# Performance work log

Measured on AMD Instinct MI355X. Metric: run time of the kernel, lower is better.

Reference implementation:

```python
import jax, jax.numpy as jnp
import numpy as np

N, H, E, T = 100000, 128, 500000, 6  # nodes, hidden, max edges, edge types


def setup_inputs() -> dict:
    key = jax.random.key(0)
    ks = jax.random.split(key, 16)
    xav_e = float(np.sqrt(6.0 / (H + T * H)))  # xavier_uniform for edge_dense
    xav_h = float(np.sqrt(6.0 / (H + H)))
    u = lambda k, s, a: jax.random.uniform(k, s, jnp.float32, -a, a)
    return {
        "node_embeddings": jax.random.normal(ks[0], (N, H), jnp.float32),
        "W_edge": u(ks[1], (H, T * H), xav_e),
        "b_edge": 1e-6 * jax.random.normal(ks[2], (T * H,), jnp.float32),
        "W_ir": u(ks[3], (H, H), xav_h), "b_ir": jnp.zeros((H,), jnp.float32),
        "W_iz": u(ks[4], (H, H), xav_h), "b_iz": jnp.zeros((H,), jnp.float32),
        "W_in": u(ks[5], (H, H), xav_h), "b_in": jnp.zeros((H,), jnp.float32),
        "W_hr": u(ks[6], (H, H), xav_h),
        "W_hz": u(ks[7], (H, H), xav_h),
        "W_hn": u(ks[8], (H, H), xav_h), "b_hn": jnp.zeros((H,), jnp.float32),
        "source_indices": jax.random.randint(ks[9], (E,), 0, N, jnp.int32),
        "dest_indices": jax.random.randint(ks[10], (E,), 0, N, jnp.int32),
        "edge_types": jax.random.randint(ks[11], (E,), 0, T, jnp.int32),
        "num_edges": 450000,
    }


def reference(node_embeddings, W_edge, b_edge, W_ir, b_ir, W_iz, b_iz,
              W_in, b_in, W_hr, W_hz, W_hn, b_hn,
              source_indices, dest_indices, edge_types, num_edges):
    num_nodes, hidden = node_embeddings.shape
    max_edges = edge_types.shape[0]
    # gather source nodes, project to all edge types at once: [E, T*H]
    src = node_embeddings[source_indices]
    all_types = (src @ W_edge + b_edge).reshape(max_edges, -1, hidden)  # [E,T,H]
    # select per-edge type
    msg = jnp.take_along_axis(all_types, edge_types[:, None, None], axis=1)[:, 0, :]
    # mask padding edges, scatter-add into destination nodes
    msg = jnp.where((jnp.arange(max_edges) < num_edges)[:, None], msg, 0)
    agg = jax.ops.segment_sum(msg, dest_indices, num_segments=num_nodes)
    # GRU update: carry h = aggregated messages, inputs x = node_embeddings
    h, x = agg, node_embeddings
    r = jax.nn.sigmoid(x @ W_ir + b_ir + h @ W_hr)
    z = jax.nn.sigmoid(x @ W_iz + b_iz + h @ W_hz)
    n = jnp.tanh(x @ W_in + b_in + r * (h @ W_hn + b_hn))
    return (1.0 - z) * n + z * h
```

## Files before the change

kernel.cpp:

```cpp
#include <hip/hip_runtime.h>
#include <hip/hip_bf16.h>

#define HD 128
#define NT 6

typedef unsigned short u16;
typedef unsigned int u32;
typedef __attribute__((ext_vector_type(8))) short bf16x8;
typedef __attribute__((ext_vector_type(4))) float f32x4;

__device__ __forceinline__ float sigmoidf_(float x) {
  return 1.0f / (1.0f + __expf(-x));
}

__device__ __forceinline__ u16 f2bf(float x) {
  u32 u = __float_as_uint(x);
  return (u16)((u + 0x7FFFu + ((u >> 16) & 1u)) >> 16);
}
__device__ __forceinline__ float bflo(u32 v) { return __uint_as_float(v << 16); }
__device__ __forceinline__ float bfhi(u32 v) { return __uint_as_float(v & 0xffff0000u); }
__device__ __forceinline__ float bfs(u16 v) { return __uint_as_float((u32)v << 16); }

__device__ __forceinline__ int swz(int p) { return p ^ (((p >> 8) & 7) << 4); }

__global__ void k_cvt_w(const float* __restrict__ We,
                        const float* __restrict__ Wir, const float* __restrict__ Wiz,
                        const float* __restrict__ Win, const float* __restrict__ Whr,
                        const float* __restrict__ Whz, const float* __restrict__ Whn,
                        u16* __restrict__ WeT, u16* __restrict__ WgT) {
  int i = blockIdx.x * blockDim.x + threadIdx.x;
  if (i < NT * HD * HD) {
    int c = i >> 7, k = i & 127;
    WeT[i] = f2bf(We[(size_t)k * (NT * HD) + c]);
  } else {
    int j = i - NT * HD * HD;
    if (j < 6 * HD * HD) {
      int m = j >> 14, jj = j & 16383;
      int c = jj >> 7, k = jj & 127;
      const float* W = (m == 0) ? Wir : (m == 1) ? Wiz : (m == 2) ? Win
                     : (m == 3) ? Whr : (m == 4) ? Whz : Whn;
      WgT[j] = f2bf(W[(size_t)k * HD + c]);
    }
  }
}

__global__ __launch_bounds__(256) void k_gemm_edge6(
    const float* __restrict__ X, const u16* __restrict__ WeT,
    const float* __restrict__ Be, u16* __restrict__ P, int N)
{
  __shared__ char As[32768];
  __shared__ char Bs[32768];
  const int tid = threadIdx.x;
  const int row0 = blockIdx.x * 128;

  #pragma unroll
  for (int i = 0; i < 8; ++i) {
    int p = i * 4096 + tid * 16;
    int row = row0 + (p >> 8);
    union { u16 u[8]; bf16x8 v; } ra;
    if (row < N) {
      const float4* s = (const float4*)(X + (size_t)row0 * HD + (p >> 1));
      float4 f0 = s[0], f1 = s[1];
      ra.u[0] = f2bf(f0.x); ra.u[1] = f2bf(f0.y); ra.u[2] = f2bf(f0.z); ra.u[3] = f2bf(f0.w);
      ra.u[4] = f2bf(f1.x); ra.u[5] = f2bf(f1.y); ra.u[6] = f2bf(f1.z); ra.u[7] = f2bf(f1.w);
    } else {
      #pragma unroll
      for (int j = 0; j < 8; ++j) ra.u[j] = 0;
    }
    *(bf16x8*)(As + swz(p)) = ra.v;
  }

  const int l = tid & 63, w = tid >> 6;
  const int m0 = (w >> 1) * 64, n0 = (w & 1) * 64;
  const int lr = l & 15, lg = l >> 4;
  f32x4 zero = {0.f, 0.f, 0.f, 0.f};

  for (int t = 0; t < NT; ++t) {
    __syncthreads();
    const char* gB = (const char*)(WeT + (size_t)t * HD * HD);
    #pragma unroll
    for (int i = 0; i < 8; ++i) {
      int p = i * 4096 + tid * 16;
      *(bf16x8*)(Bs + swz(p)) = *(const bf16x8*)(gB + p);
    }
    __syncthreads();

    f32x4 acc[4][4];
    #pragma unroll
    for (int m = 0; m < 4; ++m)
      #pragma unroll
      for (int n = 0; n < 4; ++n) acc[m][n] = zero;

    #pragma unroll
    for (int k = 0; k < 4; ++k) {
      bf16x8 a[4], b[4];
      #pragma unroll
      for (int m = 0; m < 4; ++m)
        a[m] = *(const bf16x8*)(As + swz((m0 + m * 16 + lr) * 256 + k * 64 + lg * 16));
      #pragma unroll
      for (int n = 0; n < 4; ++n)
        b[n] = *(const bf16x8*)(Bs + swz((n0 + n * 16 + lr) * 256 + k * 64 + lg * 16));
      #pragma unroll
      for (int m = 0; m < 4; ++m)
        #pragma unroll
        for (int n = 0; n < 4; ++n)
          acc[m][n] = __builtin_amdgcn_mfma_f32_16x16x32_bf16(a[m], b[n], acc[m][n], 0, 0, 0);
    }

    float bias[4];
    #pragma unroll
    for (int n = 0; n < 4; ++n) bias[n] = Be[t * HD + n0 + n * 16 + lr];
    #pragma unroll
    for (int m = 0; m < 4; ++m) {
      int rbase = row0 + m0 + m * 16 + lg * 4;
      #pragma unroll
      for (int j = 0; j < 4; ++j) {
        int row = rbase + j;
        if (row < N) {
          #pragma unroll
          for (int n = 0; n < 4; ++n)
            P[(size_t)row * (NT * HD) + t * HD + n0 + n * 16 + lr] =
                f2bf(acc[m][n][j] + bias[n]);
        }
      }
    }
  }
}

__global__ __launch_bounds__(256) void k_count(const int* __restrict__ dst,
                                               const int* __restrict__ nePtr,
                                               int* __restrict__ deg) {
  const int ne = nePtr[0];
  for (int e = blockIdx.x * blockDim.x + threadIdx.x; e < ne;
       e += gridDim.x * blockDim.x)
    atomicAdd(&deg[dst[e]], 1);
}

__global__ __launch_bounds__(256) void k_scan_a(const int* __restrict__ deg,
                                                int* __restrict__ off,
                                                int* __restrict__ bsum, int N) {
  __shared__ int s[256];
  const int b = blockIdx.x, tid = threadIdx.x;
  const int base = b * 1024 + tid * 4;
  int v0 = 0, v1 = 0, v2 = 0, v3 = 0;
  if (base < N) v0 = deg[base];
  if (base + 1 < N) v1 = deg[base + 1];
  if (base + 2 < N) v2 = deg[base + 2];
  if (base + 3 < N) v3 = deg[base + 3];
  const int sum = v0 + v1 + v2 + v3;
  s[tid] = sum;
  __syncthreads();
  for (int d = 1; d < 256; d <<= 1) {
    int t = (tid >= d) ? s[tid - d] : 0;
    __syncthreads();
    s[tid] += t;
    __syncthreads();
  }
  const int excl = s[tid] - sum;
  if (base < N) off[base] = excl;
  if (base + 1 < N) off[base + 1] = excl + v0;
  if (base + 2 < N) off[base + 2] = excl + v0 + v1;
  if (base + 3 < N) off[base + 3] = excl + v0 + v1 + v2;
  if (tid == 255) bsum[b] = s[255];
}

__global__ void k_scan_b(int* __restrict__ bsum, int nb) {
  __shared__ int s[1024];
  const int tid = threadIdx.x;
  const int v = (tid < nb) ? bsum[tid] : 0;
  s[tid] = v;
  __syncthreads();
  for (int d = 1; d < 1024; d <<= 1) {
    int t = (tid >= d) ? s[tid - d] : 0;
    __syncthreads();
    s[tid] += t;
    __syncthreads();
  }
  if (tid < nb) bsum[tid] = s[tid] - v;
}

__global__ __launch_bounds__(256) void k_scan_c(int* __restrict__ off,
                                                const int* __restrict__ bsum, int N) {
  const int b = blockIdx.x, tid = threadIdx.x;
  const int add = bsum[b];
  const int base = b * 1024 + tid * 4;
  #pragma unroll
  for (int i = 0; i < 4; ++i)
    if (base + i < N) off[base + i] += add;
}

__global__ __launch_bounds__(256) void k_fill(const int* __restrict__ src,
                                              const int* __restrict__ dst,
                                              const int* __restrict__ typ,
                                              const int* __restrict__ nePtr,
                                              int* __restrict__ off,
                                              u32* __restrict__ elist) {
  const int ne = nePtr[0];
  for (int e = blockIdx.x * blockDim.x + threadIdx.x; e < ne;
       e += gridDim.x * blockDim.x) {
    int pos = atomicAdd(&off[dst[e]], 1);
    elist[pos] = (u32)(src[e] * NT + typ[e]);
  }
}

__global__ __launch_bounds__(256) void k_gather(
    const u16* __restrict__ P, const int* __restrict__ deg,
    const int* __restrict__ off, const u32* __restrict__ elist,
    u16* __restrict__ Hb, int N)
{
  const int l = threadIdx.x & 63;
  int wid = (int)((blockIdx.x * blockDim.x + threadIdx.x) >> 6);
  int nw = (int)((gridDim.x * blockDim.x) >> 6);
  for (int n = wid; n < N; n += nw) {
    const int e1 = off[n];
    const int e0 = e1 - deg[n];
    float a0 = 0.f, a1 = 0.f, b0 = 0.f, b1 = 0.f;
    for (int e = e0; e < e1; e += 4) {
      u32 p0 = elist[e];
      u32 p1 = (e + 1 < e1) ? elist[e + 1] : p0;
      u32 p2 = (e + 2 < e1) ? elist[e + 2] : p0;
      u32 p3 = (e + 3 < e1) ? elist[e + 3] : p0;
      u32 v0 = *((const u32*)(P + (size_t)p0 * HD) + l);
      u32 v1 = *((const u32*)(P + (size_t)p1 * HD) + l);
      u32 v2 = *((const u32*)(P + (size_t)p2 * HD) + l);
      u32 v3 = *((const u32*)(P + (size_t)p3 * HD) + l);
      if (e + 1 >= e1) v1 = 0;
      if (e + 2 >= e1) v2 = 0;
      if (e + 3 >= e1) v3 = 0;
      a0 += bflo(v0); a1 += bfhi(v0);
      b0 += bflo(v1); b1 += bfhi(v1);
      a0 += bflo(v2); a1 += bfhi(v2);
      b0 += bflo(v3); b1 += bfhi(v3);
    }
    a0 += b0; a1 += b1;
    u32 hp = ((u32)f2bf(a1) << 16) | (u32)f2bf(a0);
    *((u32*)(Hb + (size_t)n * HD) + l) = hp;
  }
}

__global__ __launch_bounds__(256) void k_gru6(
    const float* __restrict__ X, const u16* __restrict__ Hb,
    const u16* __restrict__ WgT,
    const float* __restrict__ bir, const float* __restrict__ biz,
    const float* __restrict__ bin_, const float* __restrict__ bhn,
    float* __restrict__ out, int N)
{
  __shared__ char Wb[2][32768];
  const int tid = threadIdx.x;
  const int l = tid & 63, w = tid >> 6;
  const int lr = l & 15, lg = l >> 4;
  const int rw = blockIdx.x * 64 + w * 16;
  const int arow = rw + lr;

  const bf16x8 zf = {0, 0, 0, 0, 0, 0, 0, 0};
  bf16x8 Xa[4], Ha[4];
  if (arow < N) {
    #pragma unroll
    for (int kc = 0; kc < 4; ++kc) {
      const float4* sx = (const float4*)(X + (size_t)arow * HD + kc * 32 + lg * 8);
      float4 x0 = sx[0], x1 = sx[1];
      union { u16 u[8]; bf16x8 v; } rx;
      rx.u[0] = f2bf(x0.x); rx.u[1] = f2bf(x0.y); rx.u[2] = f2bf(x0.z); rx.u[3] = f2bf(x0.w);
      rx.u[4] = f2bf(x1.x); rx.u[5] = f2bf(x1.y); rx.u[6] = f2bf(x1.z); rx.u[7] = f2bf(x1.w);
      Xa[kc] = rx.v;
      Ha[kc] = *(const bf16x8*)(Hb + (size_t)arow * HD + kc * 32 + lg * 8);
    }
  } else {
    #pragma unroll
    for (int kc = 0; kc < 4; ++kc) { Xa[kc] = zf; Ha[kc] = zf; }
  }

  bf16x8 wreg[8];
  auto loadW = [&](int g) {
    const char* gp = (const char*)(WgT + (size_t)g * HD * HD);
    #pragma unroll
    for (int i = 0; i < 8; ++i)
      wreg[i] = *(const bf16x8*)(gp + i * 4096 + tid * 16);
  };
  auto writeW = [&](int buf) {
    #pragma unroll
    for (int i = 0; i < 8; ++i) {
      int p = i * 4096 + tid * 16;
      *(bf16x8*)(Wb[buf] + swz(p)) = wreg[i];
    }
  };

  f32x4 zero = {0.f, 0.f, 0.f, 0.f};
  auto sweep = [&](const bf16x8* A, int buf, f32x4* acc) {
    #pragma unroll
    for (int n = 0; n < 8; ++n) acc[n] = zero;
    #pragma unroll
    for (int kc = 0; kc < 4; ++kc) {
      #pragma unroll
      for (int n = 0; n < 8; ++n) {
        bf16x8 b = *(const bf16x8*)(Wb[buf] + swz((n * 16 + lr) * 256 + kc * 64 + lg * 16));
        acc[n] = __builtin_amdgcn_mfma_f32_16x16x32_bf16(A[kc], b, acc[n], 0, 0, 0);
      }
    }
  };

  f32x4 t1[8], t2[8], rg[8], nn[8];
  float bv[8];

  loadW(0); writeW(0);
  __syncthreads();

  loadW(3);
  sweep(Xa, 0, t1);
  writeW(1);
  __syncthreads();

  loadW(5);
  sweep(Ha, 1, t2);
  writeW(0);
  #pragma unroll
  for (int n = 0; n < 8; ++n) bv[n] = bir[n * 16 + lr];
  #pragma unroll
  for (int n = 0; n < 8; ++n)
    #pragma unroll
    for (int j = 0; j < 4; ++j) rg[n][j] = sigmoidf_(t1[n][j] + bv[n] + t2[n][j]);
  __syncthreads();

  loadW(2);
  sweep(Ha, 0, t2);
  writeW(1);
  #pragma unroll
  for (int n = 0; n < 8; ++n) bv[n] = bhn[n * 16 + lr];
  #pragma unroll
  for (int n = 0; n < 8; ++n)
    #pragma unroll
    for (int j = 0; j < 4; ++j) rg[n][j] *= (t2[n][j] + bv[n]);
  __syncthreads();

  loadW(1);
  sweep(Xa, 1, t1);
  writeW(0);
  #pragma unroll
  for (int n = 0; n < 8; ++n) bv[n] = bin_[n * 16 + lr];
  #pragma unroll
  for (int n = 0; n < 8; ++n)
    #pragma unroll
    for (int j = 0; j < 4; ++j) nn[n][j] = tanhf(t1[n][j] + bv[n] + rg[n][j]);
  __syncthreads();

  loadW(4);
  sweep(Xa, 0, t1);
  writeW(1);
  __syncthreads();

  sweep(Ha, 1, t2);
  #pragma unroll
  for (int n = 0; n < 8; ++n) bv[n] = biz[n * 16 + lr];
  #pragma unroll
  for (int n = 0; n < 8; ++n) {
    #pragma unroll
    for (int j = 0; j < 4; ++j) {
      int row = rw + lg * 4 + j;
      if (row < N) {
        int col = n * 16 + lr;
        float z = sigmoidf_(t1[n][j] + bv[n] + t2[n][j]);
        float h = bfs(Hb[(size_t)row * HD + col]);
        out[(size_t)row * HD + col] = (1.0f - z) * nn[n][j] + z * h;
      }
    }
  }
}

__global__ __launch_bounds__(256) void k_gather_gru(
    const float* __restrict__ X, const u16* __restrict__ P,
    const int* __restrict__ deg, const int* __restrict__ off,
    const u32* __restrict__ elist, const u16* __restrict__ WgT,
    const float* __restrict__ bir, const float* __restrict__ biz,
    const float* __restrict__ bin_, const float* __restrict__ bhn,
    float* __restrict__ out, int N)
{
  __shared__ char Xs[16384];
  __shared__ char Hs[16384];
  const int tid = threadIdx.x;
  const int l = tid & 63, w = tid >> 6;
  const int row0 = blockIdx.x * 64;
  const int wr0 = w * 16;

  #pragma unroll
  for (int it = 0; it < 4; ++it) {
    int chunk = it * 64 + l;
    int r = chunk >> 4, seg = chunk & 15;
    int grow = row0 + wr0 + r;
    union { u16 u[8]; bf16x8 v; } rx;
    if (grow < N) {
      const float4* sx = (const float4*)(X + (size_t)grow * HD + seg * 8);
      float4 x0 = sx[0], x1 = sx[1];
      rx.u[0] = f2bf(x0.x); rx.u[1] = f2bf(x0.y); rx.u[2] = f2bf(x0.z); rx.u[3] = f2bf(x0.w);
      rx.u[4] = f2bf(x1.x); rx.u[5] = f2bf(x1.y); rx.u[6] = f2bf(x1.z); rx.u[7] = f2bf(x1.w);
    } else {
      #pragma unroll
      for (int j = 0; j < 8; ++j) rx.u[j] = 0;
    }
    *(bf16x8*)(Xs + swz((wr0 + r) * 256 + seg * 16)) = rx.v;
  }

  for (int i = 0; i < 16; ++i) {
    int n = row0 + wr0 + i;
    float a0 = 0.f, a1 = 0.f;
    if (n < N) {
      int e1 = off[n];
      for (int e = e1 - deg[n]; e < e1; e += 4) {
        u32 p0 = elist[e];
        u32 p1 = (e + 1 < e1) ? elist[e + 1] : p0;
        u32 p2 = (e + 2 < e1) ? elist[e + 2] : p0;
        u32 p3 = (e + 3 < e1) ? elist[e + 3] : p0;
        u32 v0 = *((const u32*)(P + (size_t)p0 * HD) + l);
        u32 v1 = *((const u32*)(P + (size_t)p1 * HD) + l);
        u32 v2 = *((const u32*)(P + (size_t)p2 * HD) + l);
        u32 v3 = *((const u32*)(P + (size_t)p3 * HD) + l);
        if (e + 1 >= e1) v1 = 0;
        if (e + 2 >= e1) v2 = 0;
        if (e + 3 >= e1) v3 = 0;
        a0 += bflo(v0) + bflo(v1) + bflo(v2) + bflo(v3);
        a1 += bfhi(v0) + bfhi(v1) + bfhi(v2) + bfhi(v3);
      }
    }
    u32 hp = ((u32)f2bf(a1) << 16) | (u32)f2bf(a0);
    *(u32*)(Hs + swz((wr0 + i) * 256 + l * 4)) = hp;
  }

  const int lr = l & 15, lg = l >> 4;
  const int rloc = wr0;

  f32x4 zero = {0.f, 0.f, 0.f, 0.f};
  auto sweep = [&](const char* Ab, const u16* WT, f32x4* acc) {
    #pragma unroll
    for (int n = 0; n < 8; ++n) acc[n] = zero;
    #pragma unroll
    for (int k = 0; k < 4; ++k) {
      bf16x8 a = *(const bf16x8*)(Ab + swz((rloc + lr) * 256 + k * 64 + lg * 16));
      #pragma unroll
      for (int n = 0; n < 8; ++n) {
        bf16x8 b = *(const bf16x8*)(WT + (size_t)(n * 16 + lr) * HD + k * 32 + lg * 8);
        acc[n] = __builtin_amdgcn_mfma_f32_16x16x32_bf16(a, b, acc[n], 0, 0, 0);
      }
    }
  };

  f32x4 t1[8], t2[8], rg[8], nn[8];
  float bv[8];

  sweep(Xs, WgT + 0 * HD * HD, t1);
  sweep(Hs, WgT + 3 * HD * HD, t2);
  #pragma unroll
  for (int n = 0; n < 8; ++n) bv[n] = bir[n * 16 + lr];
  #pragma unroll
  for (int n = 0; n < 8; ++n)
    #pragma unroll
    for (int j = 0; j < 4; ++j) rg[n][j] = sigmoidf_(t1[n][j] + bv[n] + t2[n][j]);

  sweep(Hs, WgT + 5 * HD * HD, t2);
  #pragma unroll
  for (int n = 0; n < 8; ++n) bv[n] = bhn[n * 16 + lr];
  #pragma unroll
  for (int n = 0; n < 8; ++n)
    #pragma unroll
    for (int j = 0; j < 4; ++j) rg[n][j] *= (t2[n][j] + bv[n]);

  sweep(Xs, WgT + 2 * HD * HD, t1);
  #pragma unroll
  for (int n = 0; n < 8; ++n) bv[n] = bin_[n * 16 + lr];
  #pragma unroll
  for (int n = 0; n < 8; ++n)
    #pragma unroll
    for (int j = 0; j < 4; ++j) nn[n][j] = tanhf(t1[n][j] + bv[n] + rg[n][j]);

  sweep(Xs, WgT + 1 * HD * HD, t1);
  sweep(Hs, WgT + 4 * HD * HD, t2);
  #pragma unroll
  for (int n = 0; n < 8; ++n) bv[n] = biz[n * 16 + lr];
  #pragma unroll
  for (int n = 0; n < 8; ++n) {
    #pragma unroll
    for (int j = 0; j < 4; ++j) {
      int row = row0 + rloc + lg * 4 + j;
      if (row < N) {
        float z = sigmoidf_(t1[n][j] + bv[n] + t2[n][j]);
        u16 hu = *(const u16*)(Hs + swz((rloc + lg * 4 + j) * 256 + (n * 16 + lr) * 2));
        out[(size_t)row * HD + n * 16 + lr] = (1.0f - z) * nn[n][j] + z * bfs(hu);
      }
    }
  }
}

__global__ __launch_bounds__(256) void k_scatter(
    const u16* __restrict__ P, const int* __restrict__ src,
    const int* __restrict__ dst, const int* __restrict__ typ,
    const int* __restrict__ nePtr, float* __restrict__ agg,
    int ldP, int fixedType)
{
  const int ne = nePtr[0];
  const int lane = threadIdx.x & 63;
  const int wid = (int)((blockIdx.x * blockDim.x + threadIdx.x) >> 6);
  const int nw = (int)((gridDim.x * blockDim.x) >> 6);
  for (int e = wid; e < ne; e += nw) {
    const int t = typ[e];
    if (fixedType >= 0 && t != fixedType) continue;
    const size_t po = (ldP == HD) ? (size_t)src[e] * HD
                                  : (size_t)src[e] * (NT * HD) + (size_t)t * HD;
    u32 v = *(const u32*)(P + po + lane * 2);
    float* o = agg + (size_t)dst[e] * HD + lane * 2;
    unsafeAtomicAdd(o, bflo(v));
    unsafeAtomicAdd(o + 1, bfhi(v));
  }
}

__global__ __launch_bounds__(256) void k_gru(
    const float* __restrict__ X, const float* __restrict__ agg,
    const u16* __restrict__ WgT,
    const float* __restrict__ bir, const float* __restrict__ biz,
    const float* __restrict__ bin_, const float* __restrict__ bhn,
    float* __restrict__ out, int N)
{
  __shared__ char Xs[16384];
  __shared__ char Hs[16384];
  const int tid = threadIdx.x;
  const int row0 = blockIdx.x * 64;

  #pragma unroll
  for (int i = 0; i < 4; ++i) {
    int p = i * 4096 + tid * 16;
    int row = row0 + (p >> 8);
    union { u16 u[8]; bf16x8 v; } rx, rh;
    if (row < N) {
      const float4* sx = (const float4*)(X + (size_t)row0 * HD + (p >> 1));
      const float4* sh = (const float4*)(agg + (size_t)row0 * HD + (p >> 1));
      float4 x0 = sx[0], x1 = sx[1], h0 = sh[0], h1 = sh[1];
      rx.u[0] = f2bf(x0.x); rx.u[1] = f2bf(x0.y); rx.u[2] = f2bf(x0.z); rx.u[3] = f2bf(x0.w);
      rx.u[4] = f2bf(x1.x); rx.u[5] = f2bf(x1.y); rx.u[6] = f2bf(x1.z); rx.u[7] = f2bf(x1.w);
      rh.u[0] = f2bf(h0.x); rh.u[1] = f2bf(h0.y); rh.u[2] = f2bf(h0.z); rh.u[3] = f2bf(h0.w);
      rh.u[4] = f2bf(h1.x); rh.u[5] = f2bf(h1.y); rh.u[6] = f2bf(h1.z); rh.u[7] = f2bf(h1.w);
    } else {
      #pragma unroll
      for (int j = 0; j < 8; ++j) { rx.u[j] = 0; rh.u[j] = 0; }
    }
    *(bf16x8*)(Xs + swz(p)) = rx.v;
    *(bf16x8*)(Hs + swz(p)) = rh.v;
  }
  __syncthreads();

  const int l = tid & 63, w = tid >> 6;
  const int lr = l & 15, lg = l >> 4;
  const int rloc = w * 16;

  f32x4 zero = {0.f, 0.f, 0.f, 0.f};
  auto sweep = [&](const char* Ab, const u16* WT, f32x4* acc) {
    #pragma unroll
    for (int n = 0; n < 8; ++n) acc[n] = zero;
    #pragma unroll
    for (int k = 0; k < 4; ++k) {
      bf16x8 a = *(const bf16x8*)(Ab + swz((rloc + lr) * 256 + k * 64 + lg * 16));
      #pragma unroll
      for (int n = 0; n < 8; ++n) {
        bf16x8 b = *(const bf16x8*)(WT + (size_t)(n * 16 + lr) * HD + k * 32 + lg * 8);
        acc[n] = __builtin_amdgcn_mfma_f32_16x16x32_bf16(a, b, acc[n], 0, 0, 0);
      }
    }
  };

  f32x4 t1[8], t2[8], rg[8], nn[8];
  float bv[8];

  sweep(Xs, WgT + 0 * HD * HD, t1);
  sweep(Hs, WgT + 3 * HD * HD, t2);
  #pragma unroll
  for (int n = 0; n < 8; ++n) bv[n] = bir[n * 16 + lr];
  #pragma unroll
  for (int n = 0; n < 8; ++n)
    #pragma unroll
    for (int j = 0; j < 4; ++j) rg[n][j] = sigmoidf_(t1[n][j] + bv[n] + t2[n][j]);

  sweep(Hs, WgT + 5 * HD * HD, t2);
  #pragma unroll
  for (int n = 0; n < 8; ++n) bv[n] = bhn[n * 16 + lr];
  #pragma unroll
  for (int n = 0; n < 8; ++n)
    #pragma unroll
    for (int j = 0; j < 4; ++j) rg[n][j] *= (t2[n][j] + bv[n]);

  sweep(Xs, WgT + 2 * HD * HD, t1);
  #pragma unroll
  for (int n = 0; n < 8; ++n) bv[n] = bin_[n * 16 + lr];
  #pragma unroll
  for (int n = 0; n < 8; ++n)
    #pragma unroll
    for (int j = 0; j < 4; ++j) nn[n][j] = tanhf(t1[n][j] + bv[n] + rg[n][j]);

  sweep(Xs, WgT + 1 * HD * HD, t1);
  sweep(Hs, WgT + 4 * HD * HD, t2);
  #pragma unroll
  for (int n = 0; n < 8; ++n) bv[n] = biz[n * 16 + lr];
  #pragma unroll
  for (int n = 0; n < 8; ++n) {
    #pragma unroll
    for (int j = 0; j < 4; ++j) {
      int row = row0 + rloc + lg * 4 + j;
      if (row < N) {
        float z = sigmoidf_(t1[n][j] + bv[n] + t2[n][j]);
        float h = agg[(size_t)row * HD + n * 16 + lr];
        out[(size_t)row * HD + n * 16 + lr] = (1.0f - z) * nn[n][j] + z * h;
      }
    }
  }
}

extern "C" void kernel_launch(void* const* d_in, const int* in_sizes, int n_in,
                              void* d_out, int out_size, void* d_ws, size_t ws_size,
                              hipStream_t stream) {
  const float* X      = (const float*)d_in[0];
  const float* W_edge = (const float*)d_in[1];
  const float* b_edge = (const float*)d_in[2];
  const float* b_ir   = (const float*)d_in[4];
  const float* b_iz   = (const float*)d_in[6];
  const float* b_in   = (const float*)d_in[8];
  const float* b_hn   = (const float*)d_in[12];
  const int* src      = (const int*)d_in[13];
  const int* dst      = (const int*)d_in[14];
  const int* typ      = (const int*)d_in[15];
  const int* nePtr    = (const int*)d_in[16];

  const int N = in_sizes[0] / HD;
  const int E = in_sizes[13];
  char* ws = (char*)d_ws;

  size_t cur = 0;
  auto alloc = [&](size_t bytes) {
    size_t p = cur;
    cur = (cur + bytes + 255) & ~(size_t)255;
    return p;
  };
  u16* WeT   = (u16*)(ws + alloc((size_t)NT * HD * HD * 2));
  u16* WgT   = (u16*)(ws + alloc((size_t)6 * HD * HD * 2));
  int* deg   = (int*)(ws + alloc((size_t)N * 4));
  int* offA  = (int*)(ws + alloc((size_t)N * 4));
  int* bsum  = (int*)(ws + alloc(1024 * 4));
  u32* elist = (u32*)(ws + alloc((size_t)E * 4));
  size_t base_need = cur;
  u16* P     = (u16*)(ws + alloc((size_t)N * NT * HD * 2));
  const size_t csr_need = cur;
  u16* Hb    = (u16*)(ws + alloc((size_t)N * HD * 2));
  const size_t split_need = cur;

  const int gb = (N + 127) / 128;
  const int NB = (N + 1023) / 1024;

  k_cvt_w<<<(NT * HD * HD + 6 * HD * HD + 255) / 256, 256, 0, stream>>>(
      W_edge, (const float*)d_in[3], (const float*)d_in[5], (const float*)d_in[7],
      (const float*)d_in[9], (const float*)d_in[10], (const float*)d_in[11], WeT, WgT);

  if (ws_size >= csr_need) {
    hipMemsetAsync(deg, 0, (size_t)N * 4, stream);
    k_gemm_edge6<<<gb, 256, 0, stream>>>(X, WeT, b_edge, P, N);
    k_count<<<1024, 256, 0, stream>>>(dst, nePtr, deg);
    k_scan_a<<<NB, 256, 0, stream>>>(deg, offA, bsum, N);
    k_scan_b<<<1, 1024, 0, stream>>>(bsum, NB);
    k_scan_c<<<NB, 256, 0, stream>>>(offA, bsum, N);
    k_fill<<<1024, 256, 0, stream>>>(src, dst, typ, nePtr, offA, elist);
    if (ws_size >= split_need) {
      k_gather<<<(N + 3) / 4, 256, 0, stream>>>(P, deg, offA, elist, Hb, N);
      k_gru6<<<(N + 63) / 64, 256, 0, stream>>>(
          X, Hb, WgT, b_ir, b_iz, b_in, b_hn, (float*)d_out, N);
    } else {
      k_gather_gru<<<(N + 63) / 64, 256, 0, stream>>>(
          X, P, deg, offA, elist, WgT, b_ir, b_iz, b_in, b_hn, (float*)d_out, N);
    }
  } else {
    float* agg = (float*)d_out;
    hipMemsetAsync(d_out, 0, (size_t)out_size * sizeof(float), stream);
    size_t pneed = base_need + (size_t)N * NT * HD * 2;
    if (ws_size >= pneed) {
      u16* Pf = (u16*)(ws + base_need);
      k_gemm_edge6<<<gb, 256, 0, stream>>>(X, WeT, b_edge, Pf, N);
      k_scatter<<<2048, 256, 0, stream>>>(Pf, src, dst, typ, nePtr, agg, NT * HD, -1);
      k_gru<<<(N + 63) / 64, 256, 0, stream>>>(X, agg, WgT, b_ir, b_iz, b_in, b_hn, agg, N);
    }
  }
}
```

Baseline: 273.2 us.

## Split GRU into input-projection GEMM and persistent hidden-state GRU kernel

The input-side gate projections (X·W_ir/iz/in plus biases) move into a separate MFMA GEMM that writes bf16 results in fragment order into the freed P buffer. A new persistent kernel keeps all three hidden-weight matrices resident in 96KB of LDS in pre-swizzled fragment layout, so the per-block weight reload and barrier sequence of the old GRU kernel goes away. It computes the three hidden GEMMs in one interleaved loop and fuses the gate math. In exchange it adds a kernel launch, a bf16 round-trip of the input-gate activations, and large LDS use that limits occupancy.

```diff
diff --git a/kernel.cpp b/kernel.cpp
--- a/kernel.cpp
+++ b/kernel.cpp
@@ -8,6 +8,7 @@
 typedef unsigned int u32;
 typedef __attribute__((ext_vector_type(8))) short bf16x8;
 typedef __attribute__((ext_vector_type(4))) float f32x4;
+typedef __attribute__((ext_vector_type(4))) unsigned short u16x4;
 
 __device__ __forceinline__ float sigmoidf_(float x) {
   return 1.0f / (1.0f + __expf(-x));
@@ -27,20 +28,35 @@
                         const float* __restrict__ Wir, const float* __restrict__ Wiz,
                         const float* __restrict__ Win, const float* __restrict__ Whr,
                         const float* __restrict__ Whz, const float* __restrict__ Whn,
-                        u16* __restrict__ WeT, u16* __restrict__ WgT) {
+                        u16* __restrict__ WeT9, u16* __restrict__ WgT,
+                        u16* __restrict__ WgTf) {
   int i = blockIdx.x * blockDim.x + threadIdx.x;
-  if (i < NT * HD * HD) {
-    int c = i >> 7, k = i & 127;
-    WeT[i] = f2bf(We[(size_t)k * (NT * HD) + c]);
-  } else {
-    int j = i - NT * HD * HD;
-    if (j < 6 * HD * HD) {
-      int m = j >> 14, jj = j & 16383;
-      int c = jj >> 7, k = jj & 127;
-      const float* W = (m == 0) ? Wir : (m == 1) ? Wiz : (m == 2) ? Win
-                     : (m == 3) ? Whr : (m == 4) ? Whz : Whn;
-      WgT[j] = f2bf(W[(size_t)k * HD + c]);
-    }
+  if (i < 9 * HD * HD) {
+    int m = i >> 14, jj = i & 16383;
+    int c = jj >> 7, k = jj & 127;
+    float v;
+    if (m < 6) v = We[(size_t)k * (NT * HD) + m * HD + c];
+    else {
+      const float* W = (m == 6) ? Wir : (m == 7) ? Wiz : Win;
+      v = W[(size_t)k * HD + c];
+    }
+    WeT9[i] = f2bf(v);
+  } else if (i < 15 * HD * HD) {
+    int j = i - 9 * HD * HD;
+    int m = j >> 14, jj = j & 16383;
+    int c = jj >> 7, k = jj & 127;
+    const float* W = (m == 0) ? Wir : (m == 1) ? Wiz : (m == 2) ? Win
+                   : (m == 3) ? Whr : (m == 4) ? Whz : Whn;
+    WgT[j] = f2bf(W[(size_t)k * HD + c]);
+  } else if (i < 18 * HD * HD) {
+    int j = i - 15 * HD * HD;
+    int g = j >> 14;
+    int idx = j & 16383;
+    int n = idx >> 11, kc = (idx >> 9) & 3, l = (idx >> 3) & 63, jj = idx & 7;
+    int k = kc * 32 + ((l >> 4) << 3) + jj;
+    int c = (n << 4) + (l & 15);
+    const float* W = (g == 0) ? Whr : (g == 1) ? Whn : Whz;
+    WgTf[j] = f2bf(W[(size_t)k * HD + c]);
   }
 }
 
@@ -122,6 +138,91 @@
             P[(size_t)row * (NT * HD) + t * HD + n0 + n * 16 + lr] =
                 f2bf(acc[m][n][j] + bias[n]);
         }
+      }
+    }
+  }
+}
+
+__global__ __launch_bounds__(256) void k_gemm_gx(
+    const float* __restrict__ X, const u16* __restrict__ WeT9,
+    const float* __restrict__ bir, const float* __restrict__ biz,
+    const float* __restrict__ bin_,
+    u16* __restrict__ Gx, int N, int NRB)
+{
+  __shared__ char As[32768];
+  __shared__ char Bs[32768];
+  const int tid = threadIdx.x;
+  const int row0 = blockIdx.x * 128;
+
+  #pragma unroll
+  for (int i = 0; i < 8; ++i) {
+    int p = i * 4096 + tid * 16;
+    int row = row0 + (p >> 8);
+    union { u16 u[8]; bf16x8 v; } ra;
+    if (row < N) {
+      const float4* s = (const float4*)(X + (size_t)row0 * HD + (p >> 1));
+      float4 f0 = s[0], f1 = s[1];
+      ra.u[0] = f2bf(f0.x); ra.u[1] = f2bf(f0.y); ra.u[2] = f2bf(f0.z); ra.u[3] = f2bf(f0.w);
+      ra.u[4] = f2bf(f1.x); ra.u[5] = f2bf(f1.y); ra.u[6] = f2bf(f1.z); ra.u[7] = f2bf(f1.w);
+    } else {
+      #pragma unroll
+      for (int j = 0; j < 8; ++j) ra.u[j] = 0;
+    }
+    *(bf16x8*)(As + swz(p)) = ra.v;
+  }
+
+  const int l = tid & 63, w = tid >> 6;
+  const int m0 = (w >> 1) * 64, n0 = (w & 1) * 64;
+  const int lr = l & 15, lg = l >> 4;
+  f32x4 zero = {0.f, 0.f, 0.f, 0.f};
+
+  for (int t = 0; t < 3; ++t) {
+    __syncthreads();
+    const char* gB = (const char*)(WeT9 + (size_t)(6 + t) * HD * HD);
+    #pragma unroll
+    for (int i = 0; i < 8; ++i) {
+      int p = i * 4096 + tid * 16;
+      *(bf16x8*)(Bs + swz(p)) = *(const bf16x8*)(gB + p);
+    }
+    __syncthreads();
+
+    f32x4 acc[4][4];
+    #pragma unroll
+    for (int m = 0; m < 4; ++m)
+      #pragma unroll
+      for (int n = 0; n < 4; ++n) acc[m][n] = zero;
+
+    #pragma unroll
+    for (int k = 0; k < 4; ++k) {
+      bf16x8 a[4], b[4];
+      #pragma unroll
+      for (int m = 0; m < 4; ++m)
+        a[m] = *(const bf16x8*)(As + swz((m0 + m * 16 + lr) * 256 + k * 64 + lg * 16));
+      #pragma unroll
+      for (int n = 0; n < 4; ++n)
+        b[n] = *(const bf16x8*)(Bs + swz((n0 + n * 16 + lr) * 256 + k * 64 + lg * 16));
+      #pragma unroll
+      for (int m = 0; m < 4; ++m)
+        #pragma unroll
+        for (int n = 0; n < 4; ++n)
+          acc[m][n] = __builtin_amdgcn_mfma_f32_16x16x32_bf16(a[m], b[n], acc[m][n], 0, 0, 0);
+    }
+
+    const float* bp = (t == 0) ? bir : (t == 1) ? biz : bin_;
+    float bias[4];
+    #pragma unroll
+    for (int n = 0; n < 4; ++n) bias[n] = bp[n0 + n * 16 + lr];
+
+    #pragma unroll
+    for (int m = 0; m < 4; ++m) {
+      int rb = (row0 >> 4) + (w >> 1) * 4 + m;
+      #pragma unroll
+      for (int n = 0; n < 4; ++n) {
+        int np = (w & 1) * 4 + n;
+        u16x4 pk;
+        #pragma unroll
+        for (int j = 0; j < 4; ++j) pk[j] = f2bf(acc[m][n][j] + bias[n]);
+        *(u16x4*)(Gx + ((size_t)t * NRB + rb) * 2048 + (np * 64 + l) * 4) = pk;
       }
     }
   }
@@ -238,129 +339,86 @@
   }
 }
 
-__global__ __launch_bounds__(256) void k_gru6(
-    const float* __restrict__ X, const u16* __restrict__ Hb,
-    const u16* __restrict__ WgT,
-    const float* __restrict__ bir, const float* __restrict__ biz,
-    const float* __restrict__ bin_, const float* __restrict__ bhn,
-    float* __restrict__ out, int N)
+__global__ __launch_bounds__(512, 2) void k_gruH(
+    const u16* __restrict__ Hb, const u16* __restrict__ WgTf,
+    const u16* __restrict__ Gx,
+    const float* __restrict__ bhn,
+    float* __restrict__ out, int N, int NRB, int ntiles)
 {
-  __shared__ char Wb[2][32768];
+  __shared__ char Wl[98304];
   const int tid = threadIdx.x;
   const int l = tid & 63, w = tid >> 6;
   const int lr = l & 15, lg = l >> 4;
-  const int rw = blockIdx.x * 64 + w * 16;
-  const int arow = rw + lr;
+
+  #pragma unroll
+  for (int i = 0; i < 12; ++i)
+    *(bf16x8*)(Wl + i * 8192 + tid * 16) =
+        *(const bf16x8*)((const char*)WgTf + i * 8192 + tid * 16);
+  __syncthreads();
+
+  float bvn[8];
+  #pragma unroll
+  for (int n = 0; n < 8; ++n) bvn[n] = bhn[n * 16 + lr];
 
   const bf16x8 zf = {0, 0, 0, 0, 0, 0, 0, 0};
-  bf16x8 Xa[4], Ha[4];
-  if (arow < N) {
+  f32x4 zero = {0.f, 0.f, 0.f, 0.f};
+  const size_t gstride = (size_t)NRB * 2048;
+
+  for (int tile = blockIdx.x; tile < ntiles; tile += gridDim.x) {
+    const int rw = tile * 128 + w * 16;
+    const int rb = tile * 8 + w;
+    const int arow = rw + lr;
+
+    bf16x8 Ha[4];
+    if (arow < N) {
+      #pragma unroll
+      for (int kc = 0; kc < 4; ++kc)
+        Ha[kc] = *(const bf16x8*)(Hb + (size_t)arow * HD + kc * 32 + lg * 8);
+    } else {
+      #pragma unroll
+      for (int kc = 0; kc < 4; ++kc) Ha[kc] = zf;
+    }
+
+    u16x4 gr[8], gz[8], gn[8];
+    #pragma unroll
+    for (int n = 0; n < 8; ++n) {
+      size_t o = ((size_t)rb * 512 + n * 64 + l) * 4;
+      gr[n] = *(const u16x4*)(Gx + o);
+      gz[n] = *(const u16x4*)(Gx + gstride + o);
+      gn[n] = *(const u16x4*)(Gx + 2 * gstride + o);
+    }
+
+    f32x4 thr[8], thn[8], thz[8];
+    #pragma unroll
+    for (int n = 0; n < 8; ++n) { thr[n] = zero; thn[n] = zero; thz[n] = zero; }
     #pragma unroll
     for (int kc = 0; kc < 4; ++kc) {
-      const float4* sx = (const float4*)(X + (size_t)arow * HD + kc * 32 + lg * 8);
-      float4 x0 = sx[0], x1 = sx[1];
-      union { u16 u[8]; bf16x8 v; } rx;
-      rx.u[0] = f2bf(x0.x); rx.u[1] = f2bf(x0.y); rx.u[2] = f2bf(x0.z); rx.u[3] = f2bf(x0.w);
-      rx.u[4] = f2bf(x1.x); rx.u[5] = f2bf(x1.y); rx.u[6] = f2bf(x1.z); rx.u[7] = f2bf(x1.w);
-      Xa[kc] = rx.v;
-      Ha[kc] = *(const bf16x8*)(Hb + (size_t)arow * HD + kc * 32 + lg * 8);
-    }
-  } else {
-    #pragma unroll
-    for (int kc = 0; kc < 4; ++kc) { Xa[kc] = zf; Ha[kc] = zf; }
-  }
-
-  bf16x8 wreg[8];
-  auto loadW = [&](int g) {
-    const char* gp = (const char*)(WgT + (size_t)g * HD * HD);
-    #pragma unroll
-    for (int i = 0; i < 8; ++i)
-      wreg[i] = *(const bf16x8*)(gp + i * 4096 + tid * 16);
-  };
-  auto writeW = [&](int buf) {
-    #pragma unroll
-    for (int i = 0; i < 8; ++i) {
-      int p = i * 4096 + tid * 16;
-      *(bf16x8*)(Wb[buf] + swz(p)) = wreg[i];
-    }
-  };
-
-  f32x4 zero = {0.f, 0.f, 0.f, 0.f};
-  auto sweep = [&](const bf16x8* A, int buf, f32x4* acc) {
-    #pragma unroll
-    for (int n = 0; n < 8; ++n) acc[n] = zero;
-    #pragma unroll
-    for (int kc = 0; kc < 4; ++kc) {
       #pragma unroll
       for (int n = 0; n < 8; ++n) {
-        bf16x8 b = *(const bf16x8*)(Wb[buf] + swz((n * 16 + lr) * 256 + kc * 64 + lg * 16));
-        acc[n] = __builtin_amdgcn_mfma_f32_16x16x32_bf16(A[kc], b, acc[n], 0, 0, 0);
-      }
-    }
-  };
-
-  f32x4 t1[8], t2[8], rg[8], nn[8];
-  float bv[8];
-
-  loadW(0); writeW(0);
-  __syncthreads();
-
-  loadW(3);
-  sweep(Xa, 0, t1);
-  writeW(1);
-  __syncthreads();
-
-  loadW(5);
-  sweep(Ha, 1, t2);
-  writeW(0);
-  #pragma unroll
-  for (int n = 0; n < 8; ++n) bv[n] = bir[n * 16 + lr];
-  #pragma unroll
-  for (int n = 0; n < 8; ++n)
-    #pragma unroll
-    for (int j = 0; j < 4; ++j) rg[n][j] = sigmoidf_(t1[n][j] + bv[n] + t2[n][j]);
-  __syncthreads();
-
-  loadW(2);
-  sweep(Ha, 0, t2);
-  writeW(1);
-  #pragma unroll
-  for (int n = 0; n < 8; ++n) bv[n] = bhn[n * 16 + lr];
-  #pragma unroll
-  for (int n = 0; n < 8; ++n)
-    #pragma unroll
-    for (int j = 0; j < 4; ++j) rg[n][j] *= (t2[n][j] + bv[n]);
-  __syncthreads();
-
-  loadW(1);
-  sweep(Xa, 1, t1);
-  writeW(0);
-  #pragma unroll
-  for (int n = 0; n < 8; ++n) bv[n] = bin_[n * 16 + lr];
-  #pragma unroll
-  for (int n = 0; n < 8; ++n)
-    #pragma unroll
-    for (int j = 0; j < 4; ++j) nn[n][j] = tanhf(t1[n][j] + bv[n] + rg[n][j]);
-  __syncthreads();
-
-  loadW(4);
-  sweep(Xa, 0, t1);
-  writeW(1);
-  __syncthreads();
-
-  sweep(Ha, 1, t2);
-  #pragma unroll
-  for (int n = 0; n < 8; ++n) bv[n] = biz[n * 16 + lr];
-  #pragma unroll
-  for (int n = 0; n < 8; ++n) {
-    #pragma unroll
-    for (int j = 0; j < 4; ++j) {
-      int row = rw + lg * 4 + j;
-      if (row < N) {
-        int col = n * 16 + lr;
-        float z = sigmoidf_(t1[n][j] + bv[n] + t2[n][j]);
-        float h = bfs(Hb[(size_t)row * HD + col]);
-        out[(size_t)row * HD + col] = (1.0f - z) * nn[n][j] + z * h;
+        const int fo = ((n * 4 + kc) * 64 + l) * 16;
+        bf16x8 b0 = *(const bf16x8*)(Wl + fo);
+        thr[n] = __builtin_amdgcn_mfma_f32_16x16x32_bf16(Ha[kc], b0, thr[n], 0, 0, 0);
+        bf16x8 b1 = *(const bf16x8*)(Wl + 32768 + fo);
+        thn[n] = __builtin_amdgcn_mfma_f32_16x16x32_bf16(Ha[kc], b1, thn[n], 0, 0, 0);
+        bf16x8 b2 = *(const bf16x8*)(Wl + 65536 + fo);
+        thz[n] = __builtin_amdgcn_mfma_f32_16x16x32_bf16(Ha[kc], b2, thz[n], 0, 0, 0);
+      }
+    }
+
+    #pragma unroll
+    for (int n = 0; n < 8; ++n) {
+      #pragma unroll
+      for (int j = 0; j < 4; ++j) {
+        int row = rw + lg * 4 + j;
+        if (row < N) {
+          int col = n * 16 + lr;
+          float r  = sigmoidf_(bfs(gr[n][j]) + thr[n][j]);
+          float rn = r * (thn[n][j] + bvn[n]);
+          float nn = tanhf(bfs(gn[n][j]) + rn);
+          float z  = sigmoidf_(bfs(gz[n][j]) + thz[n][j]);
+          float h  = bfs(Hb[(size_t)row * HD + col]);
+          out[(size_t)row * HD + col] = (1.0f - z) * nn + z * h;
+        }
       }
     }
   }
@@ -628,54 +686,66 @@
   const int E = in_sizes[13];
   char* ws = (char*)d_ws;
 
+  const int gb = (N + 127) / 128;
+  const int NB = (N + 1023) / 1024;
+  const int NRB = gb * 8;
+
   size_t cur = 0;
   auto alloc = [&](size_t bytes) {
     size_t p = cur;
     cur = (cur + bytes + 255) & ~(size_t)255;
     return p;
   };
-  u16* WeT   = (u16*)(ws + alloc((size_t)NT * HD * HD * 2));
+  u16* WeT9  = (u16*)(ws + alloc((size_t)9 * HD * HD * 2));
   u16* WgT   = (u16*)(ws + alloc((size_t)6 * HD * HD * 2));
+  u16* WgTf  = (u16*)(ws + alloc((size_t)3 * HD * HD * 2));
   int* deg   = (int*)(ws + alloc((size_t)N * 4));
   int* offA  = (int*)(ws + alloc((size_t)N * 4));
   int* bsum  = (int*)(ws + alloc(1024 * 4));
   u32* elist = (u32*)(ws + alloc((size_t)E * 4));
   size_t base_need = cur;
-  u16* P     = (u16*)(ws + alloc((size_t)N * NT * HD * 2));
+  const size_t pBytes  = (size_t)N * NT * HD * 2;
+  const size_t gxBytes = (size_t)3 * NRB * 2048 * 2;
+  u16* P     = (u16*)(ws + alloc(pBytes > gxBytes ? pBytes : gxBytes));
   const size_t csr_need = cur;
   u16* Hb    = (u16*)(ws + alloc((size_t)N * HD * 2));
   const size_t split_need = cur;
 
-  const int gb = (N + 127) / 128;
-  const int NB = (N + 1023) / 1024;
-
-  k_cvt_w<<<(NT * HD * HD + 6 * HD * HD + 255) / 256, 256, 0, stream>>>(
+  k_cvt_w<<<(18 * HD * HD + 255) / 256, 256, 0, stream>>>(
       W_edge, (const float*)d_in[3], (const float*)d_in[5], (const float*)d_in[7],
-      (const float*)d_in[9], (const float*)d_in[10], (const float*)d_in[11], WeT, WgT);
-
-  if (ws_size >= csr_need) {
+      (const float*)d_in[9], (const float*)d_in[10], (const float*)d_in[11],
+      WeT9, WgT, WgTf);
+
+  if (ws_size >= split_need) {
     hipMemsetAsync(deg, 0, (size_t)N * 4, stream);
-    k_gemm_edge6<<<gb, 256, 0, stream>>>(X, WeT, b_edge, P, N);
+    k_gemm_edge6<<<gb, 256, 0, stream>>>(X, WeT9, b_edge, P, N);
     k_count<<<1024, 256, 0, stream>>>(dst, nePtr, deg);
     k_scan_a<<<NB, 256, 0, stream>>>(deg, offA, bsum, N);
     k_scan_b<<<1, 1024, 0, stream>>>(bsum, NB);
     k_scan_c<<<NB, 256, 0, stream>>>(offA, bsum, N);
     k_fill<<<1024, 256, 0, stream>>>(src, dst, typ, nePtr, offA, elist);
-    if (ws_size >= split_need) {
-      k_gather<<<(N + 3) / 4, 256, 0, stream>>>(P, deg, offA, elist, Hb, N);
-      k_gru6<<<(N + 63) / 64, 256, 0, stream>>>(
-          X, Hb, WgT, b_ir, b_iz, b_in, b_hn, (float*)d_out, N);
-    } else {
-      k_gather_gru<<<(N + 63) / 64, 256, 0, stream>>>(
-          X, P, deg, offA, elist, WgT, b_ir, b_iz, b_in, b_hn, (float*)d_out, N);
-    }
+    k_gather<<<(N + 3) / 4, 256, 0, stream>>>(P, deg, offA, elist, Hb, N);
+    u16* Gx = P;
+    k_gemm_gx<<<gb, 256, 0, stream>>>(X, WeT9, b_ir, b_iz, b_in, Gx, N, NRB);
+    int grid = gb < 256 ? gb : 256;
+    k_gruH<<<grid, 512, 0, stream>>>(Hb, WgTf, Gx, b_hn, (float*)d_out, N, NRB, gb);
+  } else if (ws_size >= csr_need) {
+    hipMemsetAsync(deg, 0, (size_t)N * 4, stream);
+    k_gemm_edge6<<<gb, 256, 0, stream>>>(X, WeT9, b_edge, P, N);
+    k_count<<<1024, 256, 0, stream>>>(dst, nePtr, deg);
+    k_scan_a<<<NB, 256, 0, stream>>>(deg, offA, bsum, N);
+    k_scan_b<<<1, 1024, 0, stream>>>(bsum, NB);
+    k_scan_c<<<NB, 256, 0, stream>>>(offA, bsum, N);
+    k_fill<<<1024, 256, 0, stream>>>(src, dst, typ, nePtr, offA, elist);
+    k_gather_gru<<<(N + 63) / 64, 256, 0, stream>>>(
+        X, P, deg, offA, elist, WgT, b_ir, b_iz, b_in, b_hn, (float*)d_out, N);
   } else {
     float* agg = (float*)d_out;
     hipMemsetAsync(d_out, 0, (size_t)out_size * sizeof(float), stream);
-    size_t pneed = base_need + (size_t)N * NT * HD * 2;
+    size_t pneed = base_need + pBytes;
     if (ws_size >= pneed) {
       u16* Pf = (u16*)(ws + base_need);
-      k_gemm_edge6<<<gb, 256, 0, stream>>>(X, WeT, b_edge, Pf, N);
+      k_gemm_edge6<<<gb, 256, 0, stream>>>(X, WeT9, b_edge, Pf, N);
       k_scatter<<<2048, 256, 0, stream>>>(Pf, src, dst, typ, nePtr, agg, NT * HD, -1);
       k_gru<<<(N + 63) / 64, 256, 0, stream>>>(X, agg, WgT, b_ir, b_iz, b_in, b_hn, agg, N);
     }
```

Measured after the change: 449.8 us. 1.65x slower.
